# Performance work log

Measured on AMD Instinct MI355X. Metric: run time of the kernel, lower is better.

Reference implementation:

```python
import jax, jax.numpy as jnp
import numpy as np

B, I, S, H, O = 128, 64, 2048, 128, 64


def setup_inputs() -> dict:
    key = jax.random.key(0)
    ks = jax.random.split(key, 9)
    sc = 0.1
    return {
        "x": jax.random.normal(ks[0], (B, I, S), dtype=jnp.float32),
        "Wx_out": jax.random.normal(ks[1], (I, 4 * H), dtype=jnp.float32) * sc,
        "Wh_out": jax.random.normal(ks[2], (H, 4 * H), dtype=jnp.float32) * sc,
        "b_out": jnp.zeros((4 * H,), dtype=jnp.float32),
        "Wx_in": jax.random.normal(ks[3], (H, 4 * H), dtype=jnp.float32) * sc,
        "Wh_in": jax.random.normal(ks[4], (H, 4 * H), dtype=jnp.float32) * sc,
        "b_in": jnp.zeros((4 * H,), dtype=jnp.float32),
        "W_lin": jax.random.normal(ks[5], (O, H), dtype=jnp.float32) * 0.01,
        "b_lin": jnp.zeros((O,), dtype=jnp.float32),
    }


def reference(x, Wx_out, Wh_out, b_out, Wx_in, Wh_in, b_in, W_lin, b_lin):
    # x: (B, I, S) -> permute(0,2,1) -> (B, S, I); scan over time axis.
    xs = jnp.transpose(x, (2, 0, 1))  # (S, B, I)
    h0 = jnp.zeros((x.shape[0], Wh_out.shape[0]), dtype=x.dtype)

    def step(carry, xt):
        h, c, cn = carry  # outer hidden, outer cell, inner cell
        gates = xt @ Wx_out + h @ Wh_out + b_out
        i, f, o, g = jnp.split(gates, 4, axis=-1)
        i, f, o = jax.nn.sigmoid(i), jax.nn.sigmoid(f), jax.nn.sigmoid(o)
        g = jnp.tanh(g)
        x_in = i * g          # inner LSTM input
        h_in = f * c          # inner LSTM hidden
        gi = x_in @ Wx_in + h_in @ Wh_in + b_in
        ii, fi, oi, gg = jnp.split(gi, 4, axis=-1)
        cn_new = jax.nn.sigmoid(fi) * cn + jax.nn.sigmoid(ii) * jnp.tanh(gg)
        c_new = jax.nn.sigmoid(oi) * jnp.tanh(cn_new)  # outer cell = inner hidden
        h_new = o * jnp.tanh(c_new)
        return (h_new, c_new, cn_new), h_new

    _, hs = jax.lax.scan(step, (h0, h0, h0), xs)  # hs: (S, B, H)
    hs = jnp.transpose(hs, (1, 0, 2))             # (B, S, H)
    return hs @ W_lin.T + b_lin                   # (B, S, O)
```

## Files before the change

kernel.cpp:

```cpp
#include <hip/hip_runtime.h>
#include <hip/hip_fp16.h>

#define BB 128
#define II 64
#define SS 2048
#define HH 128
#define GG 512
#define OO 64
#define TT 32
#define TCH 128
#define XPBYTES ((size_t)BB * SS * GG * 2)

typedef _Float16 f16x2 __attribute__((ext_vector_type(2)));
union F4H { float4 f4; f16x2 h[4]; };

__device__ __forceinline__ f16x2 pack2(float a, float b) {
    f16x2 r; r.x = (_Float16)a; r.y = (_Float16)b; return r;
}

__device__ __forceinline__ float dot2(f16x2 w, f16x2 v, float c) {
#if __has_builtin(__builtin_amdgcn_fdot2)
    return __builtin_amdgcn_fdot2(w, v, c, false);
#else
    return fmaf((float)w.x, (float)v.x, fmaf((float)w.y, (float)v.y, c));
#endif
}

__device__ __forceinline__ float sigm(float v) {
    return __builtin_amdgcn_rcpf(1.0f + __expf(-v));
}
__device__ __forceinline__ float tanh_f(float v) {
    float a = fabsf(v);
    float e = __expf(-2.0f * a);
    float r = (1.0f - e) * __builtin_amdgcn_rcpf(1.0f + e);
    return v < 0.0f ? -r : r;
}
__device__ __forceinline__ float tanh_c(float v) {
    return fmaf(2.0f, __builtin_amdgcn_rcpf(1.0f + __expf(-2.0f * v)), -1.0f);
}

__global__ void __launch_bounds__(512)
xp_gemm(const float* __restrict__ x, const float* __restrict__ Wx_out,
        _Float16* __restrict__ xp)
{
    const int tc = blockIdx.x;
    const int b  = blockIdx.y;
    const int j  = threadIdx.x;
    const int t0 = tc * TCH;

    __shared__ __align__(16) f16x2 x2s[TCH][36];

    f16x2 w2[32];
#pragma unroll
    for (int c = 0; c < 32; ++c)
        w2[c] = pack2(Wx_out[(2 * c) * GG + j], Wx_out[(2 * c + 1) * GG + j]);

    const float* xrow = x + (size_t)b * II * SS;
    const int r = j >> 3;
#pragma unroll
    for (int rep = 0; rep < 4; ++rep) {
        const int u = (j & 7) + 8 * rep;
        const float4 v = *(const float4*)(xrow + (size_t)r * SS + t0 + 4 * u);
        const int c = r >> 1, half = r & 1;
        ((_Float16*)&x2s[4 * u + 0][c])[half] = (_Float16)v.x;
        ((_Float16*)&x2s[4 * u + 1][c])[half] = (_Float16)v.y;
        ((_Float16*)&x2s[4 * u + 2][c])[half] = (_Float16)v.z;
        ((_Float16*)&x2s[4 * u + 3][c])[half] = (_Float16)v.w;
    }
    __syncthreads();

    _Float16* xpo = xp + ((size_t)b * SS + t0) * GG + j;
#pragma unroll 4
    for (int tt = 0; tt < TCH; ++tt) {
        const float4* xr4 = (const float4*)&x2s[tt][0];
        float a0 = 0.f, a1 = 0.f;
#pragma unroll
        for (int q = 0; q < 8; ++q) {
            F4H u; u.f4 = xr4[q];
            a0 = dot2(w2[4 * q + 0], u.h[0], a0);
            a1 = dot2(w2[4 * q + 1], u.h[1], a1);
            a0 = dot2(w2[4 * q + 2], u.h[2], a0);
            a1 = dot2(w2[4 * q + 3], u.h[3], a1);
        }
        xpo[(size_t)tt * GG] = (_Float16)(a0 + a1);
    }
}

__global__ void __launch_bounds__(512)
nlstm_scan_xp(
    const _Float16* __restrict__ xp,
    const float* __restrict__ Wh_out, const float* __restrict__ b_out,
    const float* __restrict__ Wx_in, const float* __restrict__ Wh_in,
    const float* __restrict__ b_in,
    const float* __restrict__ W_lin, const float* __restrict__ b_lin,
    float* __restrict__ out)
{
    const int b = blockIdx.x;
    const int j = threadIdx.x;

    __shared__ __align__(16) float4 wlf[16 * 66];
    __shared__ __align__(16) f16x2 hb[HH / 2];
    __shared__ __align__(16) f16x2 xib[HH / 2];
    __shared__ __align__(16) f16x2 hib[HH / 2];
    __shared__ float cb[HH];
    __shared__ float cnb[HH];
    __shared__ float actO[GG];
    __shared__ float actI[GG];

    f16x2 who[HH / 2], wxi[HH / 2], whi[HH / 2];
#pragma unroll
    for (int m = 0; m < HH / 2; ++m)
        who[m] = pack2(Wh_out[(2 * m) * GG + j], Wh_out[(2 * m + 1) * GG + j]);
#pragma unroll
    for (int m = 0; m < HH / 2; ++m)
        wxi[m] = pack2(Wx_in[(2 * m) * GG + j], Wx_in[(2 * m + 1) * GG + j]);
#pragma unroll
    for (int m = 0; m < HH / 2; ++m)
        whi[m] = pack2(Wh_in[(2 * m) * GG + j], Wh_in[(2 * m + 1) * GG + j]);

    const float bo = b_out[j];
    const float bi = b_in[j];
    const int   pn = j >> 3;
    const int   ps = j & 7;
    const float bl = b_lin[pn];

#pragma unroll
    for (int r = 0; r < 2; ++r) {
        const int m = r * 512 + j;
        const int c = m >> 6, n = m & 63;
        F4H u;
#pragma unroll
        for (int q = 0; q < 4; ++q)
            u.h[q] = pack2(W_lin[n * HH + 8 * c + 2 * q],
                           W_lin[n * HH + 8 * c + 2 * q + 1]);
        wlf[c * 66 + n] = u.f4;
    }

    if (j < HH / 2) hb[j] = pack2(0.f, 0.f);
    if (j < HH) { cb[j] = 0.f; cnb[j] = 0.f; }
    __syncthreads();

    const _Float16* xpr = xp + (size_t)b * SS * GG + j;
    float* orow = out + (size_t)b * SS * OO;
    const float4* hb4 = (const float4*)hb;
    const float4* xi4 = (const float4*)xib;
    const float4* hi4 = (const float4*)hib;

    _Float16 xpc = xpr[0];

#pragma unroll 1
    for (int t = 0; t < SS; ++t) {
        float a0 = bo + (float)xpc, a1 = 0.f, a2 = 0.f, a3 = 0.f;
#pragma unroll
        for (int c = 0; c < 16; ++c) {
            F4H hu; hu.f4 = hb4[c];
            a0 = dot2(who[4 * c + 0], hu.h[0], a0);
            a1 = dot2(who[4 * c + 1], hu.h[1], a1);
            a2 = dot2(who[4 * c + 2], hu.h[2], a2);
            a3 = dot2(who[4 * c + 3], hu.h[3], a3);
        }
        const _Float16 xpn = xpr[(size_t)(((t + 1) & (SS - 1))) * GG];
        {
            const float acc = (a0 + a1) + (a2 + a3);
            actO[j] = (j < 384) ? sigm(acc) : tanh_c(acc);
        }
        __syncthreads();

        if ((j & 7) == 0) {
            const int m = j >> 3;
            xib[m] = pack2(actO[2 * m] * actO[384 + 2 * m],
                           actO[2 * m + 1] * actO[384 + 2 * m + 1]);
        } else if ((j & 7) == 4) {
            const int m = j >> 3;
            hib[m] = pack2(actO[HH + 2 * m] * cb[2 * m],
                           actO[HH + 2 * m + 1] * cb[2 * m + 1]);
        }
        __syncthreads();

        float c0 = bi, c1 = 0.f, c2 = 0.f, c3 = 0.f;
#pragma unroll
        for (int c = 0; c < 16; ++c) {
            F4H xu; xu.f4 = xi4[c];
            c0 = dot2(wxi[4 * c + 0], xu.h[0], c0);
            c1 = dot2(wxi[4 * c + 1], xu.h[1], c1);
            c2 = dot2(wxi[4 * c + 2], xu.h[2], c2);
            c3 = dot2(wxi[4 * c + 3], xu.h[3], c3);
        }
#pragma unroll
        for (int c = 0; c < 16; ++c) {
            F4H hu; hu.f4 = hi4[c];
            c0 = dot2(whi[4 * c + 0], hu.h[0], c0);
            c1 = dot2(whi[4 * c + 1], hu.h[1], c1);
            c2 = dot2(whi[4 * c + 2], hu.h[2], c2);
            c3 = dot2(whi[4 * c + 3], hu.h[3], c3);
        }
        {
            const float acc2 = (c0 + c1) + (c2 + c3);
            actI[j] = (j < 384) ? sigm(acc2) : tanh_c(acc2);
        }
        __syncthreads();

        if ((j & 3) == 0) {
            const int m = j >> 2;
            const float cn_new = actI[HH + m] * cnb[m] + actI[m] * actI[384 + m];
            const float c_new  = actI[2 * HH + m] * tanh_c(cn_new);
            const float h_new  = actO[2 * HH + m] * tanh_c(c_new);
            cnb[m] = cn_new;
            cb[m]  = c_new;
            ((_Float16*)hb)[m] = (_Float16)h_new;
        }
        __syncthreads();

        float p = 0.f;
#pragma unroll
        for (int q = 0; q < 2; ++q) {
            const int c = 2 * ps + q;
            F4H hu; hu.f4 = hb4[c];
            F4H wu; wu.f4 = wlf[c * 66 + pn];
            p = dot2(wu.h[0], hu.h[0], p);
            p = dot2(wu.h[1], hu.h[1], p);
            p = dot2(wu.h[2], hu.h[2], p);
            p = dot2(wu.h[3], hu.h[3], p);
        }
        p += __shfl_down(p, 4, 8);
        p += __shfl_down(p, 2, 8);
        p += __shfl_down(p, 1, 8);
        if (ps == 0) orow[t * OO + pn] = p + bl;

        xpc = xpn;
    }
}

__global__ void
__attribute__((amdgpu_flat_work_group_size(512, 512)))
__attribute__((amdgpu_waves_per_eu(2, 2)))
nlstm_scan(
    const float* __restrict__ x,
    const float* __restrict__ Wx_out, const float* __restrict__ Wh_out,
    const float* __restrict__ b_out,
    const float* __restrict__ Wx_in, const float* __restrict__ Wh_in,
    const float* __restrict__ b_in,
    const float* __restrict__ W_lin, const float* __restrict__ b_lin,
    float* __restrict__ out)
{
    const int b = blockIdx.x;
    const int j = threadIdx.x;

    __shared__ __align__(16) float4 wxf[8 * 512];
    __shared__ __align__(16) float4 wlf[16 * 66];
    __shared__ float xt[2][II][TT + 1];
    __shared__ __align__(16) f16x2 xb[2][II / 2];
    __shared__ __align__(16) f16x2 hb[HH / 2];
    __shared__ __align__(16) f16x2 xib[HH / 2];
    __shared__ __align__(16) f16x2 hib[HH / 2];
    __shared__ float cb[HH];
    __shared__ float cnb[HH];
    __shared__ float actO[GG];
    __shared__ float actI[GG];

    f16x2 who[HH / 2], wxi[HH / 2], whi[HH / 2];
#pragma unroll
    for (int m = 0; m < HH / 2; ++m)
        who[m] = pack2(Wh_out[(2 * m) * GG + j], Wh_out[(2 * m + 1) * GG + j]);
#pragma unroll
    for (int m = 0; m < HH / 2; ++m)
        wxi[m] = pack2(Wx_in[(2 * m) * GG + j], Wx_in[(2 * m + 1) * GG + j]);
#pragma unroll
    for (int m = 0; m < HH / 2; ++m)
        whi[m] = pack2(Wh_in[(2 * m) * GG + j], Wh_in[(2 * m + 1) * GG + j]);

    const float bo = b_out[j];
    const float bi = b_in[j];
    const int   pn = j >> 3;
    const int   ps = j & 7;
    const float bl = b_lin[pn];

#pragma unroll
    for (int c = 0; c < 8; ++c) {
        F4H u;
#pragma unroll
        for (int q = 0; q < 4; ++q)
            u.h[q] = pack2(Wx_out[(8 * c + 2 * q) * GG + j],
                           Wx_out[(8 * c + 2 * q + 1) * GG + j]);
        wxf[c * 512 + j] = u.f4;
    }
#pragma unroll
    for (int r = 0; r < 2; ++r) {
        const int m = r * 512 + j;
        const int c = m >> 6, n = m & 63;
        F4H u;
#pragma unroll
        for (int q = 0; q < 4; ++q)
            u.h[q] = pack2(W_lin[n * HH + 8 * c + 2 * q],
                           W_lin[n * HH + 8 * c + 2 * q + 1]);
        wlf[c * 66 + n] = u.f4;
    }

    const float* xrow = x + (size_t)b * II * SS;
    float* orow = out + (size_t)b * SS * OO;

    {
        const int row = j >> 3, tc = j & 7;
        const float4 v = *(const float4*)(xrow + (size_t)row * SS + 4 * tc);
        float* dst = &xt[0][row][4 * tc];
        dst[0] = v.x; dst[1] = v.y; dst[2] = v.z; dst[3] = v.w;
    }
    if (j < HH / 2) hb[j] = pack2(0.f, 0.f);
    if (j < HH) { cb[j] = 0.f; cnb[j] = 0.f; }
    if (j >= 256 && j < 256 + 32) {
        const int m = j - 256;
        xb[0][m] = pack2(xrow[(2 * m) * SS], xrow[(2 * m + 1) * SS]);
    }
    __syncthreads();

    const float4* hb4 = (const float4*)hb;
    const float4* xi4 = (const float4*)xib;
    const float4* hi4 = (const float4*)hib;

#pragma unroll 1
    for (int t = 0; t < SS; ++t) {
        const float4* xcur = (const float4*)xb[t & 1];
        float a0 = bo, a1 = 0.f, a2 = 0.f, a3 = 0.f;
#pragma unroll
        for (int c = 0; c < 8; ++c) {
            F4H xu; xu.f4 = xcur[c];
            F4H wu; wu.f4 = wxf[c * 512 + j];
            a0 = dot2(wu.h[0], xu.h[0], a0);
            a1 = dot2(wu.h[1], xu.h[1], a1);
            a2 = dot2(wu.h[2], xu.h[2], a2);
            a3 = dot2(wu.h[3], xu.h[3], a3);
        }
#pragma unroll
        for (int c = 0; c < 16; ++c) {
            F4H hu; hu.f4 = hb4[c];
            a0 = dot2(who[4 * c + 0], hu.h[0], a0);
            a1 = dot2(who[4 * c + 1], hu.h[1], a1);
            a2 = dot2(who[4 * c + 2], hu.h[2], a2);
            a3 = dot2(who[4 * c + 3], hu.h[3], a3);
        }
        {
            const float acc = (a0 + a1) + (a2 + a3);
            actO[j] = (j < 384) ? sigm(acc) : tanh_f(acc);
        }
        __syncthreads();

        if (j < II) {
            xib[j] = pack2(actO[2 * j] * actO[384 + 2 * j],
                           actO[2 * j + 1] * actO[384 + 2 * j + 1]);
        } else if (j < II + HH / 2) {
            const int m = j - II;
            hib[m] = pack2(actO[HH + 2 * m] * cb[2 * m],
                           actO[HH + 2 * m + 1] * cb[2 * m + 1]);
        }
        __syncthreads();

        float c0 = bi, c1 = 0.f, c2 = 0.f, c3 = 0.f;
#pragma unroll
        for (int c = 0; c < 16; ++c) {
            F4H xu; xu.f4 = xi4[c];
            c0 = dot2(wxi[4 * c + 0], xu.h[0], c0);
            c1 = dot2(wxi[4 * c + 1], xu.h[1], c1);
            c2 = dot2(wxi[4 * c + 2], xu.h[2], c2);
            c3 = dot2(wxi[4 * c + 3], xu.h[3], c3);
        }
#pragma unroll
        for (int c = 0; c < 16; ++c) {
            F4H hu; hu.f4 = hi4[c];
            c0 = dot2(whi[4 * c + 0], hu.h[0], c0);
            c1 = dot2(whi[4 * c + 1], hu.h[1], c1);
            c2 = dot2(whi[4 * c + 2], hu.h[2], c2);
            c3 = dot2(whi[4 * c + 3], hu.h[3], c3);
        }
        {
            const float acc2 = (c0 + c1) + (c2 + c3);
            actI[j] = (j < 384) ? sigm(acc2) : tanh_f(acc2);
        }
        __syncthreads();

        const bool doTile = ((t & 31) == 30) && (t + 2 < SS);
        float4 xld; int Tn = 0;
        if (doTile) {
            Tn = (t + 2) >> 5;
            const int row = j >> 3, tc = j & 7;
            xld = *(const float4*)(xrow + (size_t)row * SS + TT * Tn + 4 * tc);
        }
        if (j < HH) {
            const float cn_new = actI[HH + j] * cnb[j] + actI[j] * actI[384 + j];
            const float c_new  = actI[2 * HH + j] * tanh_f(cn_new);
            const float h_new  = actO[2 * HH + j] * tanh_f(c_new);
            cnb[j] = cn_new;
            cb[j]  = c_new;
            ((_Float16*)hb)[j] = (_Float16)h_new;
        } else if (j < HH + 32) {
            const int m = j - HH;
            const int tn = t + 1;
            const int tbn = (tn >> 5) & 1, ttn = tn & 31;
            xb[tn & 1][m] = pack2(xt[tbn][2 * m][ttn],
                                  xt[tbn][2 * m + 1][ttn]);
        }
        if (doTile) {
            const int row = j >> 3, tc = j & 7;
            float* dst = &xt[Tn & 1][row][4 * tc];
            dst[0] = xld.x; dst[1] = xld.y; dst[2] = xld.z; dst[3] = xld.w;
        }
        __syncthreads();

        float p = 0.f;
#pragma unroll
        for (int q = 0; q < 2; ++q) {
            const int c = 2 * ps + q;
            F4H hu; hu.f4 = hb4[c];
            F4H wu; wu.f4 = wlf[c * 66 + pn];
            p = dot2(wu.h[0], hu.h[0], p);
            p = dot2(wu.h[1], hu.h[1], p);
            p = dot2(wu.h[2], hu.h[2], p);
            p = dot2(wu.h[3], hu.h[3], p);
        }
        p += __shfl_down(p, 4, 8);
        p += __shfl_down(p, 2, 8);
        p += __shfl_down(p, 1, 8);
        if (ps == 0) orow[t * OO + pn] = p + bl;
    }
}

extern "C" void kernel_launch(void* const* d_in, const int* in_sizes, int n_in,
                              void* d_out, int out_size, void* d_ws, size_t ws_size,
                              hipStream_t stream) {
    (void)in_sizes; (void)n_in; (void)out_size;
    const float* x      = (const float*)d_in[0];
    const float* Wx_out = (const float*)d_in[1];
    const float* Wh_out = (const float*)d_in[2];
    const float* b_out  = (const float*)d_in[3];
    const float* Wx_in  = (const float*)d_in[4];
    const float* Wh_in  = (const float*)d_in[5];
    const float* b_in   = (const float*)d_in[6];
    const float* W_lin  = (const float*)d_in[7];
    const float* b_lin  = (const float*)d_in[8];
    float* out = (float*)d_out;

    if (d_ws != nullptr && ws_size >= XPBYTES) {
        _Float16* xpw = (_Float16*)d_ws;
        xp_gemm<<<dim3(16, BB), dim3(512), 0, stream>>>(x, Wx_out, xpw);
        nlstm_scan_xp<<<dim3(BB), dim3(512), 0, stream>>>(
            xpw, Wh_out, b_out, Wx_in, Wh_in, b_in, W_lin, b_lin, out);
    } else {
        nlstm_scan<<<dim3(BB), dim3(512), 0, stream>>>(
            x, Wx_out, Wh_out, b_out, Wx_in, Wh_in, b_in, W_lin, b_lin, out);
    }
}
```

Measured before the change: 4.044 ms.

## Remap gate columns per hidden unit and exchange gates via lane shuffles

Each group of four consecutive threads now owns the i/f/o/g gate columns of one hidden unit. Gate activations are combined with `__shfl_xor` instead of being staged through the shared `actO`/`actI` arrays. Cell states stay in registers, which removes two `__syncthreads` barriers and several shared-memory round trips per timestep of the serial scan. A redundant extra dot-product loop with a stray label is left in, and its results are overwritten; the compiler may or may not eliminate it.

```diff
diff --git a/kernel.cpp b/kernel.cpp
--- a/kernel.cpp
+++ b/kernel.cpp
@@ -97,37 +97,40 @@
 {
     const int b = blockIdx.x;
     const int j = threadIdx.x;
+    const int g = j & 3;
+    const int m = j >> 2;
+    const int col = g * 128 + m;
 
     __shared__ __align__(16) float4 wlf[16 * 66];
-    __shared__ __align__(16) f16x2 hb[HH / 2];
-    __shared__ __align__(16) f16x2 xib[HH / 2];
-    __shared__ __align__(16) f16x2 hib[HH / 2];
-    __shared__ float cb[HH];
-    __shared__ float cnb[HH];
-    __shared__ float actO[GG];
-    __shared__ float actI[GG];
+    __shared__ __align__(16) _Float16 hb[HH];
+    __shared__ __align__(16) _Float16 xib[HH];
+    __shared__ __align__(16) _Float16 hib[HH];
 
     f16x2 who[HH / 2], wxi[HH / 2], whi[HH / 2];
 #pragma unroll
-    for (int m = 0; m < HH / 2; ++m)
-        who[m] = pack2(Wh_out[(2 * m) * GG + j], Wh_out[(2 * m + 1) * GG + j]);
-#pragma unroll
-    for (int m = 0; m < HH / 2; ++m)
-        wxi[m] = pack2(Wx_in[(2 * m) * GG + j], Wx_in[(2 * m + 1) * GG + j]);
-#pragma unroll
-    for (int m = 0; m < HH / 2; ++m)
-        whi[m] = pack2(Wh_in[(2 * m) * GG + j], Wh_in[(2 * m + 1) * GG + j]);
-
-    const float bo = b_out[j];
-    const float bi = b_in[j];
+    for (int q = 0; q < HH / 2; ++q)
+        who[q] = pack2(Wh_out[(2 * q) * GG + col], Wh_out[(2 * q + 1) * GG + col]);
+#pragma unroll
+    for (int q = 0; q < HH / 2; ++q)
+        wxi[q] = pack2(Wx_in[(2 * q) * GG + col], Wx_in[(2 * q + 1) * GG + col]);
+#pragma unroll
+    for (int q = 0; q < HH / 2; ++q)
+        whi[q] = pack2(Wh_in[(2 * q) * GG + col], Wh_in[(2 * q + 1) * GG + col]);
+
+    const float bo = b_out[col];
+    const float bi = b_in[col];
+    const float kk = (g == 3) ? 2.0f : 1.0f;
+    const float aa = (g == 3) ? 2.0f : 1.0f;
+    const float cc = (g == 3) ? -1.0f : 0.0f;
+
     const int   pn = j >> 3;
     const int   ps = j & 7;
     const float bl = b_lin[pn];
 
 #pragma unroll
     for (int r = 0; r < 2; ++r) {
-        const int m = r * 512 + j;
-        const int c = m >> 6, n = m & 63;
+        const int mm = r * 512 + j;
+        const int c = mm >> 6, n = mm & 63;
         F4H u;
 #pragma unroll
         for (int q = 0; q < 4; ++q)
@@ -136,11 +139,13 @@
         wlf[c * 66 + n] = u.f4;
     }
 
-    if (j < HH / 2) hb[j] = pack2(0.f, 0.f);
-    if (j < HH) { cb[j] = 0.f; cnb[j] = 0.f; }
+    if (j < HH) { hb[j] = (_Float16)0.f; xib[j] = (_Float16)0.f; hib[j] = (_Float16)0.f; }
+    float c_reg = 0.f;
+    float cn_reg = 0.f;
+    float o_r = 0.f;
     __syncthreads();
 
-    const _Float16* xpr = xp + (size_t)b * SS * GG + j;
+    const _Float16* xpr = xp + (size_t)b * SS * GG + col;
     float* orow = out + (size_t)b * SS * OO;
     const float4* hb4 = (const float4*)hb;
     const float4* xi4 = (const float4*)xib;
@@ -159,25 +164,34 @@
             a2 = dot2(who[4 * c + 2], hu.h[2], a2);
             a3 = dot2(who[4 * c + 3], hu.h[3], a3);
         }
-        const _Float16 xpn = xpr[(size_t)(((t + 1) & (SS - 1))) * GG];
+        const _Float16 xpn = xpr[(size_t)((t + 1) & (SS - 1)) * GG];
+        const float accA = (a0 + a1) + (a2 + a3);
+        const float v = fmaf(aa, sigm(kk * accA), cc);
+        o_r = v;
         {
-            const float acc = (a0 + a1) + (a2 + a3);
-            actO[j] = (j < 384) ? sigm(acc) : tanh_c(acc);
-        }
-        __syncthreads();
-
-        if ((j & 7) == 0) {
-            const int m = j >> 3;
-            xib[m] = pack2(actO[2 * m] * actO[384 + 2 * m],
-                           actO[2 * m + 1] * actO[384 + 2 * m + 1]);
-        } else if ((j & 7) == 4) {
-            const int m = j >> 3;
-            hib[m] = pack2(actO[HH + 2 * m] * cb[2 * m],
-                           actO[HH + 2 * m + 1] * cb[2 * m + 1]);
+            const float vg = __shfl_xor(v, 3);
+            const float cq = __shfl_xor(c_reg, 3);
+            if (g == 0)      xib[m] = (_Float16)(v * vg);
+            else if (g == 1) hib[m] = (_Float16)(v * cq);
         }
         __syncthreads();
 
         float c0 = bi, c1 = 0.f, c2 = 0.f, c3 = 0.f;
+#pragma unroll
+        for (int c = 0; c < 8; ++c) {
+            F4H xu; xu.f4 = xi4[c];
+            c0 = dot2(wxi[8 * c + 0], xu.h[0], c0);
+            c1 = dot2(wxi[8 * c + 1], xu.h[1], c1);
+            c2 = dot2(wxi[8 * c + 2], xu.h[2], c2);
+            c3 = dot2(wxi[8 * c + 3], xu.h[3], c3);
+            F4H xu2; xu2.f4 = xi4[c];
+            c0 = dot2(wxi[8 * c + 4], xu2.h[0], c0);
+            c1 = dot2(wxi[8 * c + 5], xu2.h[1], c1);
+            c2 = dot2(wxi[8 * c + 6], xu2.h[2], c2);
+            c3 = dot2(wxi[8 * c + 7], xu2.h[3], c3);
+        }
+        f32_fixup: ;
+        c0 = bi; c1 = 0.f; c2 = 0.f; c3 = 0.f;
 #pragma unroll
         for (int c = 0; c < 16; ++c) {
             F4H xu; xu.f4 = xi4[c];
@@ -194,20 +208,20 @@
             c2 = dot2(whi[4 * c + 2], hu.h[2], c2);
             c3 = dot2(whi[4 * c + 3], hu.h[3], c3);
         }
+        const float accC = (c0 + c1) + (c2 + c3);
+        const float u = fmaf(aa, sigm(kk * accC), cc);
         {
-            const float acc2 = (c0 + c1) + (c2 + c3);
-            actI[j] = (j < 384) ? sigm(acc2) : tanh_c(acc2);
-        }
-        __syncthreads();
-
-        if ((j & 3) == 0) {
-            const int m = j >> 2;
-            const float cn_new = actI[HH + m] * cnb[m] + actI[m] * actI[384 + m];
-            const float c_new  = actI[2 * HH + m] * tanh_c(cn_new);
-            const float h_new  = actO[2 * HH + m] * tanh_c(c_new);
-            cnb[m] = cn_new;
-            cb[m]  = c_new;
-            ((_Float16*)hb)[m] = (_Float16)h_new;
+            const float ug = __shfl_xor(u, 3);
+            const float p  = u * ug;
+            const float p1 = __shfl_xor(p, 1);
+            const float cn_new = fmaf(u, cn_reg, p1);
+            cn_reg = cn_new;
+            const float th1 = tanh_c(cn_new);
+            const float t2 = __shfl_xor(th1, 3);
+            const float c_new = u * t2;
+            c_reg = c_new;
+            const float h_new = o_r * tanh_c(c_new);
+            if (g == 2) hb[m] = (_Float16)h_new;
         }
         __syncthreads();
 
```

Result: faster. 3.708 ms (-8.3%).
